# Performance work log

Measured on AMD Instinct MI355X. Metric: run time of the kernel, lower is better.

## Reference

```python
import jax, jax.numpy as jnp
import numpy as np
from jax import lax

BASE_LOWER, BASE_UPPER = 0.05, 0.2
WINDOW_SIZES = (11, 25, 49)
DN = ('NCHW', 'OIHW', 'NCHW')


def _conv3x3(x, w, b):
    y = lax.conv_general_dilated(x, w, (1, 1), [(1, 1), (1, 1)], dimension_numbers=DN)
    return y + b[None, :, None, None]


def _leaky(x):
    return jnp.where(x >= 0, x, 0.2 * x)


def _std_map(feats, ws):
    # box-filter local mean / mean-of-square via depthwise conv (same math as per-channel loop)
    N, C, H, W = feats.shape
    pad = ws // 2
    fp = jnp.pad(feats, ((0, 0), (0, 0), (pad, pad), (pad, pad)), mode='reflect')
    k = jnp.ones((C, 1, ws, ws), feats.dtype) / (ws * ws)
    mean = lax.conv_general_dilated(fp, k, (1, 1), 'VALID', dimension_numbers=DN, feature_group_count=C)
    mean_sq = lax.conv_general_dilated(fp * fp, k, (1, 1), 'VALID', dimension_numbers=DN, feature_group_count=C)
    var = jnp.clip(mean_sq - mean * mean, 1e-6, None)
    cw = jax.nn.softmax(jnp.ones((C,), feats.dtype))  # C=8 -> uniform 1/8
    res = jnp.sum(jnp.sqrt(var) * cw[None, :, None, None], axis=1, keepdims=True)  # [N,1,H,W]
    return jnp.power(res, 0.8)


def _segmented_sigmoid(ns):
    low = jax.nn.sigmoid(10.0 * ns - 1.5) * 0.4
    mid = jax.nn.sigmoid(20.0 * ns - 8.0) * 0.5 + 0.25
    high = jax.nn.sigmoid(8.0 * ns - 1.0) * 0.3 + 0.7
    return jnp.where(ns < 0.25, low, jnp.where(ns <= 0.6, mid, high))


def _forward(x, w1, b1, w2, b2, w3, b3, wf, bf, channel_weights):
    # feature extractor: 4->32->16->8
    f = _conv3x3(x, w1, b1)
    f = _leaky(f)
    f = _conv3x3(f, w2, b2)
    f = _leaky(f)
    f = _conv3x3(f, w3, b3)  # [B,8,H,W]

    maps = [_std_map(f, ws) for ws in WINDOW_SIZES]
    multi = jnp.concatenate(maps, axis=1)  # [B,3,H,W]
    fused = lax.conv_general_dilated(multi, wf, (1, 1), 'VALID', dimension_numbers=DN) + bf[None, :, None, None]
    fused = jnp.maximum(fused, 0.0)  # [B,1,H,W]

    # adaptive thresholds (torch.std -> ddof=1)
    g_std = jnp.std(x, axis=(2, 3), keepdims=True, ddof=1)
    g_fac = jnp.clip(g_std * 5.0, 0.5, 2.0)
    lt = BASE_LOWER * g_fac
    ut = BASE_UPPER * g_fac
    cw = jax.nn.softmax(channel_weights).reshape(1, -1, 1, 1)
    c_std = jnp.std(x * cw, axis=(2, 3), keepdims=True, ddof=1)
    c_fac = jnp.clip(c_std * 2.0, 0.8, 1.2)
    lt = lt * c_fac  # [B,4,1,1]
    ut = ut * c_fac

    # mask generation
    q_low = jnp.quantile(fused.reshape(-1), 0.3)
    q_high = jnp.quantile(fused.reshape(-1), 0.7)
    l_mean = jnp.mean(lt, axis=1, keepdims=True)
    u_mean = jnp.mean(ut, axis=1, keepdims=True)
    l_th = (l_mean + q_low) / 2
    u_th = (u_mean + q_high) / 2
    u_th = jnp.where(u_th - l_th < 0.01, l_th + 0.01, u_th)
    ns = jnp.clip((fused - l_th) / (u_th - l_th), 0.0, 1.0)
    return _segmented_sigmoid(ns)


def setup_inputs() -> dict:
    key = jax.random.key(0)
    ks = jax.random.split(key, 8)
    B, C, H, W = 1, 4, 1536, 1536
    x = jax.random.normal(ks[0], (B, C, H, W), jnp.float32)
    w1 = jax.random.normal(ks[1], (32, 4, 3, 3), jnp.float32) * 0.1
    b1 = jax.random.normal(ks[2], (32,), jnp.float32) * 0.01
    w2 = jax.random.normal(ks[3], (16, 32, 3, 3), jnp.float32) * 0.1
    b2 = jax.random.normal(ks[4], (16,), jnp.float32) * 0.01
    w3 = jax.random.normal(ks[5], (8, 16, 3, 3), jnp.float32) * 0.1
    b3 = jax.random.normal(ks[6], (8,), jnp.float32) * 0.01
    wf = jnp.full((1, 3, 1, 1), 1.0 / 3.0, jnp.float32)  # scale_fusion init
    bf = jnp.zeros((1,), jnp.float32)
    channel_weights = jnp.ones((4,), jnp.float32) / 4.0
    return {"x": x, "w1": w1, "b1": b1, "w2": w2, "b2": b2, "w3": w3, "b3": b3,
            "wf": wf, "bf": bf, "channel_weights": channel_weights}


def reference(x, w1, b1, w2, b2, w3, b3, wf, bf, channel_weights):
    return _forward(x, w1, b1, w2, b2, w3, b3, wf, bf, channel_weights)
```

## Files before the change

kernel.cpp:

```cpp
#include <hip/hip_runtime.h>
#include <math.h>

#define HH 1536
#define WW 1536
#define HWSZ (HH*WW)

typedef __attribute__((ext_vector_type(8))) short bf16x8;
typedef __attribute__((ext_vector_type(4))) float f32x4;
#define MFMA16 __builtin_amdgcn_mfma_f32_16x16x32_bf16

struct Scalars {
  float gsum[4];
  float gsumsq[4];
};

#define OFF_F3    0UL
#define OFF_FUSED 75497472UL
#define OFF_SC    84934656UL
#define OFF_GHA   (OFF_SC + 1024UL)
#define OFF_GHB   (OFF_GHA + 2048UL*4UL)
#define OFF_GHC   (OFF_GHB + 4UL*2048UL*4UL)
#define OFF_WP    (OFF_GHC + 4UL*1024UL*4UL)
#define WS_NEEDED (OFF_WP + 38UL*512UL*2UL)

__device__ __forceinline__ short f2bf(float f) {
  unsigned u = __float_as_uint(f);
  unsigned r = (u + 0x7FFFu + ((u >> 16) & 1u)) >> 16;
  return (short)(unsigned short)r;
}
__device__ __forceinline__ float bf2f(short s) {
  return __uint_as_float(((unsigned)(unsigned short)s) << 16);
}
__device__ __forceinline__ void tsplit(float v, short &h, short &l) {
  unsigned u = __float_as_uint(v);
  h = (short)(u >> 16);
  float r = v - __uint_as_float(u & 0xffff0000u);
  l = (short)(__float_as_uint(r) >> 16);
}
__device__ __forceinline__ float leaky_f(float v) { return v >= 0.f ? v : 0.2f*v; }

__global__ __launch_bounds__(256) void k_pack(const float* __restrict__ w1,
    const float* __restrict__ w2, const float* __restrict__ w3, short* __restrict__ wp) {
  int idx = blockIdx.x*256 + threadIdx.x;
  if (idx >= 38*512) return;
  int blk = idx >> 9, e = idx & 511;
  int oc = e >> 5, k = e & 31;
  float v = 0.f; int plane = 0;
  if (blk < 8) {
    plane = blk & 1; int sl = (blk >> 1) & 1, half = blk >> 2;
    int pos = sl*8 + (k >> 2), ic = k & 3;
    if (pos < 9) v = w1[((16*half + oc)*4 + ic)*9 + pos];
  } else if (blk < 28) {
    int t = blk - 8; plane = t & 1; int hs = t >> 1;
    int half = hs / 5, sl = hs % 5;
    int p = k >> 4, icl = k & 15;
    int pos = 2*sl + p;
    if (pos < 9) v = w2[(oc*32 + half*16 + icl)*9 + pos];
  } else {
    int t = blk - 28; plane = t & 1; int sl = t >> 1;
    int pos = 2*sl + (k >> 4), ic = k & 15;
    if (oc < 8 && pos < 9) v = w3[(oc*16 + ic)*9 + pos];
  }
  short h = f2bf(v);
  wp[idx] = plane ? f2bf(v - bf2f(h)) : h;
}

__global__ __launch_bounds__(256, 3) void k_conv(
    const float* __restrict__ x,
    const float* __restrict__ b1, const float* __restrict__ b2, const float* __restrict__ b3,
    const short* __restrict__ wp, float* __restrict__ f3, Scalars* __restrict__ sc)
{
  __shared__ __align__(16) short smem[23168];
  __shared__ float red[32];
  short* f1h  = smem;
  short* f1l  = smem + 6400;
  short* xs_h = smem + 12800;
  short* xs_l = smem + 14736;
  short* f2h  = smem + 12800;
  short* f2l  = smem + 17984;

  const int tid  = threadIdx.x;
  const int lane = tid & 63;
  const int wv   = tid >> 6;
  const int pl   = lane & 15;
  const int g    = lane >> 4;
  const int x0 = blockIdx.x * 16, y0 = blockIdx.y * 16;

  float st[8];
  #pragma unroll
  for (int k = 0; k < 8; ++k) st[k] = 0.f;
  for (int i = tid; i < 484; i += 256) {
    int ry = i / 22, rx = i % 22;
    int gy = y0 - 3 + ry, gx = x0 - 3 + rx;
    bool ok = ((unsigned)gy < HH) && ((unsigned)gx < WW);
    bool interior = (ry >= 3) && (ry < 19) && (rx >= 3) && (rx < 19);
    int off = gy*WW + gx;
    short4 hv, lv;
    #pragma unroll
    for (int ic = 0; ic < 4; ++ic) {
      float v = ok ? x[ic*HWSZ + off] : 0.f;
      if (interior) { st[ic*2] += v; st[ic*2+1] += v*v; }
      short h, l; tsplit(v, h, l);
      ((short*)&hv)[ic] = h;
      ((short*)&lv)[ic] = l;
    }
    *(short4*)&xs_h[i*4] = hv;
    *(short4*)&xs_l[i*4] = lv;
  }
  #pragma unroll
  for (int k = 0; k < 8; ++k) {
    for (int o = 32; o; o >>= 1) st[k] += __shfl_down(st[k], o, 64);
  }
  if (lane == 0) {
    #pragma unroll
    for (int k = 0; k < 8; ++k) red[wv*8 + k] = st[k];
  }
  __syncthreads();
  if (tid < 8) {
    float t = red[tid] + red[8+tid] + red[16+tid] + red[24+tid];
    int ch = tid >> 1;
    if (tid & 1) atomicAdd(&sc->gsumsq[ch], t);
    else         atomicAdd(&sc->gsum[ch],   t);
  }

  int c1ry[7], c1rx[7];
  #pragma unroll
  for (int n = 0; n < 7; ++n) {
    int G = wv + 4*n; if (G > 24) G = 24;
    int px = 16*G + pl;
    c1ry[n] = px / 20; c1rx[n] = px % 20;
  }
  int ryA[6], rxA[6];
  #pragma unroll
  for (int n = 0; n < 6; ++n) {
    int G = wv + 4*n; if (G > 20) G = 20;
    int px = 16*G + pl; if (px > 323) px = 323;
    ryA[n] = px / 18; rxA[n] = px % 18;
  }

  f32x4 acc2[6];
  {
    float4 bb = *(const float4*)&b2[4*g];
    #pragma unroll
    for (int n = 0; n < 6; ++n) acc2[n] = f32x4{bb.x, bb.y, bb.z, bb.w};
  }

  auto conv1_half = [&](int half) {
    f32x4 acc[7];
    float4 bb = *(const float4*)&b1[16*half + 4*g];
    #pragma unroll
    for (int n = 0; n < 7; ++n) acc[n] = f32x4{bb.x, bb.y, bb.z, bb.w};
    for (int sl = 0; sl < 2; ++sl) {
      const short* wb = wp + (size_t)((half*2 + sl)*2)*512;
      bf16x8 wh = *(const bf16x8*)(wb + pl*32 + 8*g);
      bf16x8 wl = *(const bf16x8*)(wb + 512 + pl*32 + 8*g);
      if (sl == 0) {
        int p0 = 2*g, p1 = 2*g + 1;
        int dy0 = p0/3, dx0 = p0%3, dy1 = p1/3, dx1 = p1%3;
        #pragma unroll
        for (int n = 0; n < 7; ++n) {
          int i0 = (c1ry[n] + dy0)*22 + c1rx[n] + dx0;
          int i1 = (c1ry[n] + dy1)*22 + c1rx[n] + dx1;
          short4 h0 = *(const short4*)&xs_h[i0*4];
          short4 h1 = *(const short4*)&xs_h[i1*4];
          short4 l0 = *(const short4*)&xs_l[i0*4];
          short4 l1 = *(const short4*)&xs_l[i1*4];
          bf16x8 bh = {h0.x,h0.y,h0.z,h0.w,h1.x,h1.y,h1.z,h1.w};
          bf16x8 bl = {l0.x,l0.y,l0.z,l0.w,l1.x,l1.y,l1.z,l1.w};
          acc[n] = MFMA16(wh, bh, acc[n], 0,0,0);
          acc[n] = MFMA16(wh, bl, acc[n], 0,0,0);
          acc[n] = MFMA16(wl, bh, acc[n], 0,0,0);
        }
      } else {
        #pragma unroll
        for (int n = 0; n < 7; ++n) {
          short4 h8 = {0,0,0,0}, l8 = {0,0,0,0};
          if (g == 0) {
            int i8 = (c1ry[n] + 2)*22 + c1rx[n] + 2;
            h8 = *(const short4*)&xs_h[i8*4];
            l8 = *(const short4*)&xs_l[i8*4];
          }
          bf16x8 bh = {h8.x,h8.y,h8.z,h8.w,0,0,0,0};
          bf16x8 bl = {l8.x,l8.y,l8.z,l8.w,0,0,0,0};
          acc[n] = MFMA16(wh, bh, acc[n], 0,0,0);
          acc[n] = MFMA16(wh, bl, acc[n], 0,0,0);
          acc[n] = MFMA16(wl, bh, acc[n], 0,0,0);
        }
      }
    }
    #pragma unroll
    for (int n = 0; n < 7; ++n) {
      int G = wv + 4*n; if (G > 24) G = 24;
      int px = 16*G + pl;
      int gy = y0 - 2 + c1ry[n], gx = x0 - 2 + c1rx[n];
      bool ok = ((unsigned)gy < HH) && ((unsigned)gx < WW);
      short4 hv, lv;
      #pragma unroll
      for (int r = 0; r < 4; ++r) {
        float v = ok ? leaky_f(acc[n][r]) : 0.f;
        short h, l; tsplit(v, h, l);
        ((short*)&hv)[r] = h;
        ((short*)&lv)[r] = l;
      }
      int fo = (g>>1)*3200 + px*8 + (g&1)*4;
      *(short4*)&f1h[fo] = hv;
      *(short4*)&f1l[fo] = lv;
    }
  };

  auto conv2_part = [&](int half) {
    for (int s = 0; s < 5; ++s) {
      const short* wb = wp + (size_t)(8 + (half*5 + s)*2)*512;
      bf16x8 wh = *(const bf16x8*)(wb + pl*32 + 8*g);
      bf16x8 wl = *(const bf16x8*)(wb + 512 + pl*32 + 8*g);
      int pos = 2*s + (g >> 1);
      bool pv = pos < 9;
      int dy = pv ? pos/3 : 0, dx = pv ? pos%3 : 0;
      const int pb = (g&1)*3200;
      #pragma unroll
      for (int n = 0; n < 6; ++n) {
        int idx = (ryA[n] + dy)*20 + rxA[n] + dx;
        bf16x8 bh = {0,0,0,0,0,0,0,0}, bl = {0,0,0,0,0,0,0,0};
        if (pv) {
          int so = pb + idx*8;
          bh = *(const bf16x8*)&f1h[so];
          bl = *(const bf16x8*)&f1l[so];
        }
        acc2[n] = MFMA16(wh, bh, acc2[n], 0,0,0);
        acc2[n] = MFMA16(wh, bl, acc2[n], 0,0,0);
        acc2[n] = MFMA16(wl, bh, acc2[n], 0,0,0);
      }
    }
  };

  conv1_half(0);
  __syncthreads();
  conv2_part(0);
  __syncthreads();
  conv1_half(1);
  __syncthreads();
  conv2_part(1);
  #pragma unroll
  for (int n = 0; n < 6; ++n) {
    int G = wv + 4*n; if (G > 20) G = 20;
    int px = 16*G + pl;
    if (px < 324) {
      int gy = y0 - 1 + ryA[n], gx = x0 - 1 + rxA[n];
      bool ok = ((unsigned)gy < HH) && ((unsigned)gx < WW);
      short4 hv, lv;
      #pragma unroll
      for (int r = 0; r < 4; ++r) {
        float v = ok ? leaky_f(acc2[n][r]) : 0.f;
        short h, l; tsplit(v, h, l);
        ((short*)&hv)[r] = h;
        ((short*)&lv)[r] = l;
      }
      int fo = (g>>1)*2592 + px*8 + (g&1)*4;
      *(short4*)&f2h[fo] = hv;
      *(short4*)&f2l[fo] = lv;
    }
  }
  __syncthreads();

  {
    f32x4 acc[4];
    float4 bb;
    if (g < 2) bb = *(const float4*)&b3[4*g];
    else { bb.x = 0.f; bb.y = 0.f; bb.z = 0.f; bb.w = 0.f; }
    #pragma unroll
    for (int n = 0; n < 4; ++n) acc[n] = f32x4{bb.x, bb.y, bb.z, bb.w};
    for (int s = 0; s < 5; ++s) {
      const short* wb = wp + (size_t)(28 + s*2)*512;
      bf16x8 wh = *(const bf16x8*)(wb + pl*32 + 8*g);
      bf16x8 wl = *(const bf16x8*)(wb + 512 + pl*32 + 8*g);
      int pos = 2*s + (g >> 1);
      bool pv = pos < 9;
      int dy = pv ? pos/3 : 0, dx = pv ? pos%3 : 0;
      const int pb = (g&1)*2592;
      #pragma unroll
      for (int n = 0; n < 4; ++n) {
        int px = 16*(wv + 4*n) + pl;
        int ry = px >> 4, rx = px & 15;
        int idx = (ry + dy)*18 + rx + dx;
        bf16x8 bh = {0,0,0,0,0,0,0,0}, bl = {0,0,0,0,0,0,0,0};
        if (pv) {
          int so = pb + idx*8;
          bh = *(const bf16x8*)&f2h[so];
          bl = *(const bf16x8*)&f2l[so];
        }
        acc[n] = MFMA16(wh, bh, acc[n], 0,0,0);
        acc[n] = MFMA16(wh, bl, acc[n], 0,0,0);
        acc[n] = MFMA16(wl, bh, acc[n], 0,0,0);
      }
    }
    #pragma unroll
    for (int n = 0; n < 4; ++n) {
      int px = 16*(wv + 4*n) + pl;
      int ry = px >> 4, rx = px & 15;
      size_t base = (size_t)(y0 + ry)*WW + (x0 + rx);
      #pragma unroll
      for (int r = 0; r < 4; ++r) {
        int oc = 4*g + r;
        if (oc < 8) f3[(size_t)oc*HWSZ + base] = acc[n][r];
      }
    }
  }
}

#define SATW 82
__device__ __forceinline__ float satv(const float* __restrict__ S, int r, int c) {
  return (r < 0 || c < 0) ? 0.f : S[r*SATW + c];
}
__device__ __forceinline__ float boxsum(const float* __restrict__ S, int r1, int r2, int c1, int c2) {
  return satv(S, r2, c2) - satv(S, r1-1, c2) - satv(S, r2, c1-1) + satv(S, r1-1, c1-1);
}

__global__ __launch_bounds__(256) void k_std(
    const float* __restrict__ f3, const float* __restrict__ wf,
    const float* __restrict__ bfp, float* __restrict__ fused, unsigned* __restrict__ ghA)
{
  __shared__ __align__(8) float S1[80*SATW];
  __shared__ __align__(8) float S2[80*SATW];
  const int tid = threadIdx.x;
  const int x0 = blockIdx.x * 32, y0 = blockIdx.y * 32;

  int off[25];
  #pragma unroll
  for (int it = 0; it < 25; ++it) {
    const int idx = tid + 256*it;
    const int r = idx / 80, cc = idx - r*80;
    int gy = y0 - 24 + r;  gy = gy < 0 ? -gy : (gy >= HH ? 2*HH - 2 - gy : gy);
    int gx = x0 - 24 + cc; gx = gx < 0 ? -gx : (gx >= WW ? 2*WW - 2 - gx : gx);
    off[it] = gy*WW + gx;
  }

  float pf[25];
  #pragma unroll
  for (int it = 0; it < 25; ++it) pf[it] = f3[off[it]];

  float acc0[4], acc1[4], acc2[4];
  #pragma unroll
  for (int k = 0; k < 4; ++k) { acc0[k] = 0.f; acc1[k] = 0.f; acc2[k] = 0.f; }

  for (int ch = 0; ch < 8; ++ch) {
    #pragma unroll
    for (int it = 0; it < 25; ++it) {
      const int idx = tid + 256*it;
      const int si = idx + 2*(idx/80);
      const float v = pf[it];
      S1[si] = v;
      S2[si] = v*v;
    }
    __syncthreads();
    if (ch < 7) {
      const float* fn = f3 + (size_t)(ch+1)*HWSZ;
      #pragma unroll
      for (int it = 0; it < 25; ++it) pf[it] = fn[off[it]];
    }
    if (tid < 160) {
      float* row = (tid >= 80 ? S2 + (tid-80)*SATW : S1 + tid*SATW);
      float run = 0.f;
      #pragma unroll
      for (int q = 0; q < 40; ++q) {
        float2 v = *(float2*)&row[q*2];
        float a = run + v.x;
        float b = a + v.y;
        float2 st = {a, b};
        *(float2*)&row[q*2] = st;
        run = b;
      }
    }
    __syncthreads();
    if (tid < 160) {
      float* Sc = (tid >= 80 ? S2 + (tid-80) : S1 + tid);
      float run = 0.f;
      #pragma unroll
      for (int g4 = 0; g4 < 20; ++g4) {
        float v0 = Sc[(g4*4+0)*SATW];
        float v1 = Sc[(g4*4+1)*SATW];
        float v2 = Sc[(g4*4+2)*SATW];
        float v3 = Sc[(g4*4+3)*SATW];
        run += v0; Sc[(g4*4+0)*SATW] = run;
        run += v1; Sc[(g4*4+1)*SATW] = run;
        run += v2; Sc[(g4*4+2)*SATW] = run;
        run += v3; Sc[(g4*4+3)*SATW] = run;
      }
    }
    __syncthreads();
    #pragma unroll
    for (int k = 0; k < 4; ++k) {
      const int px = tid + 256*k;
      const int py = px >> 5, xx = px & 31;
      {
        const float invn = 1.f/121.f;
        const float s1 = boxsum(S1, py+19, py+29, xx+19, xx+29);
        const float s2 = boxsum(S2, py+19, py+29, xx+19, xx+29);
        const float m = s1*invn;
        acc0[k] += sqrtf(fmaxf(s2*invn - m*m, 1e-6f));
      }
      {
        const float invn = 1.f/625.f;
        const float s1 = boxsum(S1, py+12, py+36, xx+12, xx+36);
        const float s2 = boxsum(S2, py+12, py+36, xx+12, xx+36);
        const float m = s1*invn;
        acc1[k] += sqrtf(fmaxf(s2*invn - m*m, 1e-6f));
      }
      {
        const float invn = 1.f/2401.f;
        const float s1 = boxsum(S1, py, py+48, xx, xx+48);
        const float s2 = boxsum(S2, py, py+48, xx, xx+48);
        const float m = s1*invn;
        acc2[k] += sqrtf(fmaxf(s2*invn - m*m, 1e-6f));
      }
    }
    __syncthreads();
  }

  unsigned* lh = (unsigned*)S1;
  for (int i = tid; i < 2048; i += 256) lh[i] = 0;
  __syncthreads();
  const float wv0 = wf[0], wv1 = wf[1], wv2 = wf[2], bv = bfp[0];
  #pragma unroll
  for (int k = 0; k < 4; ++k) {
    const int px = tid + 256*k;
    const int py = px >> 5, xx = px & 31;
    const float r0 = acc0[k]*0.125f, r1 = acc1[k]*0.125f, r2 = acc2[k]*0.125f;
    const float p0 = exp2f(0.8f*log2f(r0));
    const float p1 = exp2f(0.8f*log2f(r1));
    const float p2 = exp2f(0.8f*log2f(r2));
    float f = wv0*p0 + wv1*p1 + wv2*p2 + bv;
    f = fmaxf(f, 0.f);
    fused[(size_t)(y0 + py)*WW + (x0 + xx)] = f;
    atomicAdd(&lh[__float_as_uint(f) >> 21], 1u);
  }
  __syncthreads();
  for (int i = tid; i < 2048; i += 256) if (lh[i]) atomicAdd(&ghA[i], lh[i]);
}

__device__ bool scan_select(const unsigned* __restrict__ hist, int per, unsigned rank,
                            unsigned& bin, unsigned& inner) {
  const int lane = threadIdx.x & 63;
  const int base = lane * per;
  unsigned s = 0;
  for (int j = 0; j < per; ++j) s += hist[base + j];
  unsigned v = s;
  for (int off = 1; off < 64; off <<= 1) {
    unsigned n = __shfl_up(v, off, 64);
    if (lane >= off) v += n;
  }
  const unsigned excl = v - s;
  const bool has = (rank >= excl) && (rank < v);
  const unsigned long long m = __ballot(has);
  const int L = __ffsll(m) - 1;
  if (lane == L) {
    unsigned rem = rank - excl;
    for (int j = 0; j < per; ++j) {
      const unsigned c = hist[base + j];
      if (rem < c) { bin = (unsigned)(base + j); inner = rem; return true; }
      rem -= c;
    }
  }
  return false;
}

__global__ __launch_bounds__(256) void k_histB(const float* __restrict__ fused,
    const unsigned* __restrict__ ghA, unsigned* __restrict__ gh,
    unsigned r0, unsigned r1, unsigned r2, unsigned r3) {
  __shared__ unsigned lh[4*2048];
  __shared__ unsigned t1s[4];
  {
    const int w = threadIdx.x >> 6;
    const unsigned rk = (w == 0) ? r0 : (w == 1) ? r1 : (w == 2) ? r2 : r3;
    unsigned bin, inner;
    if (scan_select(ghA, 32, rk, bin, inner)) t1s[w] = bin;
  }
  for (int i = threadIdx.x; i < 8192; i += 256) lh[i] = 0;
  __syncthreads();
  const unsigned t0 = t1s[0], t1 = t1s[1], t2 = t1s[2], t3 = t1s[3];
  for (int i = blockIdx.x*256 + threadIdx.x; i < HWSZ; i += 512*256) {
    const unsigned u = __float_as_uint(fused[i]);
    const unsigned p = u >> 21, b = (u >> 10) & 2047u;
    if (p == t0) atomicAdd(&lh[b], 1u);
    if (p == t1) atomicAdd(&lh[2048 + b], 1u);
    if (p == t2) atomicAdd(&lh[4096 + b], 1u);
    if (p == t3) atomicAdd(&lh[6144 + b], 1u);
  }
  __syncthreads();
  for (int i = threadIdx.x; i < 8192; i += 256) if (lh[i]) atomicAdd(&gh[i], lh[i]);
}

__global__ __launch_bounds__(256) void k_histC(const float* __restrict__ fused,
    const unsigned* __restrict__ ghA, const unsigned* __restrict__ ghB,
    unsigned* __restrict__ gh, unsigned r0, unsigned r1, unsigned r2, unsigned r3) {
  __shared__ unsigned lh[4*1024];
  __shared__ unsigned t1s[4], in1s[4], t2s[4];
  const int w = threadIdx.x >> 6;
  {
    const unsigned rk = (w == 0) ? r0 : (w == 1) ? r1 : (w == 2) ? r2 : r3;
    unsigned bin, inner;
    if (scan_select(ghA, 32, rk, bin, inner)) { t1s[w] = bin; in1s[w] = inner; }
  }
  __syncthreads();
  {
    unsigned bin, inner;
    if (scan_select(ghB + w*2048, 32, in1s[w], bin, inner))
      t2s[w] = (t1s[w] << 11) | bin;
  }
  for (int i = threadIdx.x; i < 4096; i += 256) lh[i] = 0;
  __syncthreads();
  const unsigned t0 = t2s[0], t1 = t2s[1], t2 = t2s[2], t3 = t2s[3];
  for (int i = blockIdx.x*256 + threadIdx.x; i < HWSZ; i += 512*256) {
    const unsigned u = __float_as_uint(fused[i]);
    const unsigned p = u >> 10, b = u & 1023u;
    if (p == t0) atomicAdd(&lh[b], 1u);
    if (p == t1) atomicAdd(&lh[1024 + b], 1u);
    if (p == t2) atomicAdd(&lh[2048 + b], 1u);
    if (p == t3) atomicAdd(&lh[3072 + b], 1u);
  }
  __syncthreads();
  for (int i = threadIdx.x; i < 4096; i += 256) if (lh[i]) atomicAdd(&gh[i], lh[i]);
}

__device__ __forceinline__ float seg_sig(float ns) {
  ns = fminf(fmaxf(ns, 0.f), 1.f);
  float res;
  if (ns < 0.25f)      res = 0.4f / (1.f + expf(-(10.f*ns - 1.5f)));
  else if (ns <= 0.6f) res = 0.5f / (1.f + expf(-(20.f*ns - 8.f))) + 0.25f;
  else                 res = 0.3f / (1.f + expf(-(8.f*ns - 1.f))) + 0.7f;
  return res;
}

__global__ __launch_bounds__(256) void k_apply(const float* __restrict__ fused,
    const Scalars* __restrict__ sc, const float* __restrict__ cwp,
    const unsigned* __restrict__ ghA, const unsigned* __restrict__ ghB,
    const unsigned* __restrict__ ghC, float* __restrict__ out,
    unsigned r0, unsigned r1, unsigned r2, unsigned r3, float fr_lo, float fr_hi) {
  __shared__ unsigned t1s[4], in1s[4], t2s[4], in2s[4];
  __shared__ float vqs[4];
  __shared__ float ths[2];
  const int w = threadIdx.x >> 6;
  {
    const unsigned rk = (w == 0) ? r0 : (w == 1) ? r1 : (w == 2) ? r2 : r3;
    unsigned bin, inner;
    if (scan_select(ghA, 32, rk, bin, inner)) { t1s[w] = bin; in1s[w] = inner; }
  }
  __syncthreads();
  {
    unsigned bin, inner;
    if (scan_select(ghB + w*2048, 32, in1s[w], bin, inner)) {
      t2s[w] = (t1s[w] << 11) | bin; in2s[w] = inner;
    }
  }
  __syncthreads();
  {
    unsigned bin, inner;
    if (scan_select(ghC + w*1024, 16, in2s[w], bin, inner))
      vqs[w] = __uint_as_float((t2s[w] << 10) | bin);
  }
  __syncthreads();
  if (threadIdx.x == 0) {
    const float v0 = vqs[0], v1 = vqs[1], v2 = vqs[2], v3 = vqs[3];
    const float q_low  = v0 + fr_lo * (v1 - v0);
    const float q_high = v2 + fr_hi * (v3 - v2);
    const float c0 = cwp[0], c1 = cwp[1], c2 = cwp[2], c3 = cwp[3];
    const float mx = fmaxf(fmaxf(c0, c1), fmaxf(c2, c3));
    const float e0 = expf(c0 - mx), e1 = expf(c1 - mx), e2 = expf(c2 - mx), e3 = expf(c3 - mx);
    const float es = e0 + e1 + e2 + e3;
    const float cw[4] = {e0/es, e1/es, e2/es, e3/es};
    const double N = (double)HWSZ;
    float lsum = 0.f, usum = 0.f;
    for (int c = 0; c < 4; ++c) {
      double var = ((double)sc->gsumsq[c] - (double)sc->gsum[c]*(double)sc->gsum[c]/N) / (N - 1.0);
      if (var < 0.0) var = 0.0;
      const float gs = (float)sqrt(var);
      const float gf = fminf(fmaxf(gs*5.f, 0.5f), 2.f);
      float lt = 0.05f*gf, ut = 0.2f*gf;
      const float cs = cw[c]*gs;
      const float cf = fminf(fmaxf(cs*2.f, 0.8f), 1.2f);
      lt *= cf; ut *= cf;
      lsum += lt; usum += ut;
    }
    float l_th = 0.5f*(lsum*0.25f + q_low);
    float u_th = 0.5f*(usum*0.25f + q_high);
    if (u_th - l_th < 0.01f) u_th = l_th + 0.01f;
    ths[0] = l_th; ths[1] = u_th;
  }
  __syncthreads();
  const float l = ths[0], u = ths[1];
  const float d = u - l;
  const int i = blockIdx.x*256 + threadIdx.x;
  if (i < HWSZ/4) {
    const float4 v = ((const float4*)fused)[i];
    float4 r;
    r.x = seg_sig((v.x - l) / d);
    r.y = seg_sig((v.y - l) / d);
    r.z = seg_sig((v.z - l) / d);
    r.w = seg_sig((v.w - l) / d);
    ((float4*)out)[i] = r;
  }
}

extern "C" void kernel_launch(void* const* d_in, const int* in_sizes, int n_in,
                              void* d_out, int out_size, void* d_ws, size_t ws_size,
                              hipStream_t stream) {
  const float* x  = (const float*)d_in[0];
  const float* w1 = (const float*)d_in[1];
  const float* b1 = (const float*)d_in[2];
  const float* w2 = (const float*)d_in[3];
  const float* b2 = (const float*)d_in[4];
  const float* w3 = (const float*)d_in[5];
  const float* b3 = (const float*)d_in[6];
  const float* wf = (const float*)d_in[7];
  const float* bf = (const float*)d_in[8];
  const float* cw = (const float*)d_in[9];
  char* ws = (char*)d_ws;
  if (ws_size < WS_NEEDED) return;

  float*    f3    = (float*)(ws + OFF_F3);
  float*    fused = (float*)(ws + OFF_FUSED);
  Scalars*  sc    = (Scalars*)(ws + OFF_SC);
  unsigned* ghA   = (unsigned*)(ws + OFF_GHA);
  unsigned* ghB   = (unsigned*)(ws + OFF_GHB);
  unsigned* ghC   = (unsigned*)(ws + OFF_GHC);
  short*    wp    = (short*)(ws + OFF_WP);

  hipMemsetAsync(ws + OFF_SC, 0, OFF_WP - OFF_SC, stream);

  const double p_lo = 0.3 * (double)(HWSZ - 1);
  const double p_hi = 0.7 * (double)(HWSZ - 1);
  const unsigned k0 = (unsigned)p_lo, k1 = (unsigned)p_hi;
  const float fr_lo = (float)(p_lo - (double)k0);
  const float fr_hi = (float)(p_hi - (double)k1);

  k_pack <<<76, 256, 0, stream>>>(w1, w2, w3, wp);
  k_conv <<<dim3(96, 96), 256, 0, stream>>>(x, b1, b2, b3, wp, f3, sc);
  k_std  <<<dim3(48, 48), 256, 0, stream>>>(f3, wf, bf, fused, ghA);
  k_histB<<<512, 256, 0, stream>>>(fused, ghA, ghB, k0, k0 + 1, k1, k1 + 1);
  k_histC<<<512, 256, 0, stream>>>(fused, ghA, ghB, ghC, k0, k0 + 1, k1, k1 + 1);
  k_apply<<<(HWSZ/4 + 255)/256, 256, 0, stream>>>(fused, sc, cw, ghA, ghB, ghC,
      (float*)d_out, k0, k0 + 1, k1, k1 + 1, fr_lo, fr_hi);
}
```

Measured before the change: 483.4 us.

## Use a single shared SAT buffer in k_std, processing squares then values sequentially

The std-map kernel now keeps one 80x82 summed-area table in shared memory instead of two. For each channel it first builds the SAT of squared values, reads the three box sums into registers, then rebuilds the table from plain values to get the means. Shared memory per block is halved, and the 25-register prefetch of the next channel is dropped, which could allow more blocks per CU. In exchange each channel does two global gathers, twice as many scan passes with only 80 active threads, and more barriers, and loads are no longer overlapped with compute.

After: 672.9 us. 39.2% more time.

```diff
diff --git a/kernel.cpp b/kernel.cpp
--- a/kernel.cpp
+++ b/kernel.cpp
@@ -315,12 +315,44 @@
   return satv(S, r2, c2) - satv(S, r1-1, c2) - satv(S, r2, c1-1) + satv(S, r1-1, c1-1);
 }
 
+__device__ __forceinline__ void sat_scan(float* __restrict__ S, int tid) {
+  if (tid < 80) {
+    float* row = S + tid*SATW;
+    float run = 0.f;
+    #pragma unroll
+    for (int q = 0; q < 40; ++q) {
+      float2 v = *(float2*)&row[q*2];
+      float a = run + v.x;
+      float b = a + v.y;
+      float2 st = {a, b};
+      *(float2*)&row[q*2] = st;
+      run = b;
+    }
+  }
+  __syncthreads();
+  if (tid < 80) {
+    float* Sc = S + tid;
+    float run = 0.f;
+    #pragma unroll
+    for (int g4 = 0; g4 < 20; ++g4) {
+      float v0 = Sc[(g4*4+0)*SATW];
+      float v1 = Sc[(g4*4+1)*SATW];
+      float v2 = Sc[(g4*4+2)*SATW];
+      float v3 = Sc[(g4*4+3)*SATW];
+      run += v0; Sc[(g4*4+0)*SATW] = run;
+      run += v1; Sc[(g4*4+1)*SATW] = run;
+      run += v2; Sc[(g4*4+2)*SATW] = run;
+      run += v3; Sc[(g4*4+3)*SATW] = run;
+    }
+  }
+  __syncthreads();
+}
+
 __global__ __launch_bounds__(256) void k_std(
     const float* __restrict__ f3, const float* __restrict__ wf,
     const float* __restrict__ bfp, float* __restrict__ fused, unsigned* __restrict__ ghA)
 {
-  __shared__ __align__(8) float S1[80*SATW];
-  __shared__ __align__(8) float S2[80*SATW];
+  __shared__ __align__(8) float S[80*SATW];
   const int tid = threadIdx.x;
   const int x0 = blockIdx.x * 32, y0 = blockIdx.y * 32;
 
@@ -334,89 +366,63 @@
     off[it] = gy*WW + gx;
   }
 
-  float pf[25];
-  #pragma unroll
-  for (int it = 0; it < 25; ++it) pf[it] = f3[off[it]];
-
   float acc0[4], acc1[4], acc2[4];
   #pragma unroll
   for (int k = 0; k < 4; ++k) { acc0[k] = 0.f; acc1[k] = 0.f; acc2[k] = 0.f; }
 
   for (int ch = 0; ch < 8; ++ch) {
+    const float* fc = f3 + (size_t)ch * HWSZ;
     #pragma unroll
     for (int it = 0; it < 25; ++it) {
       const int idx = tid + 256*it;
       const int si = idx + 2*(idx/80);
-      const float v = pf[it];
-      S1[si] = v;
-      S2[si] = v*v;
+      const float v = fc[off[it]];
+      S[si] = v*v;
     }
     __syncthreads();
-    if (ch < 7) {
-      const float* fn = f3 + (size_t)(ch+1)*HWSZ;
-      #pragma unroll
-      for (int it = 0; it < 25; ++it) pf[it] = fn[off[it]];
-    }
-    if (tid < 160) {
-      float* row = (tid >= 80 ? S2 + (tid-80)*SATW : S1 + tid*SATW);
-      float run = 0.f;
-      #pragma unroll
-      for (int q = 0; q < 40; ++q) {
-        float2 v = *(float2*)&row[q*2];
-        float a = run + v.x;
-        float b = a + v.y;
-        float2 st = {a, b};
-        *(float2*)&row[q*2] = st;
-        run = b;
-      }
+    sat_scan(S, tid);
+    float q0[4], q1[4], q2[4];
+    #pragma unroll
+    for (int k = 0; k < 4; ++k) {
+      const int px = tid + 256*k;
+      const int py = px >> 5, xx = px & 31;
+      q0[k] = boxsum(S, py+19, py+29, xx+19, xx+29);
+      q1[k] = boxsum(S, py+12, py+36, xx+12, xx+36);
+      q2[k] = boxsum(S, py,    py+48, xx,    xx+48);
     }
     __syncthreads();
-    if (tid < 160) {
-      float* Sc = (tid >= 80 ? S2 + (tid-80) : S1 + tid);
-      float run = 0.f;
-      #pragma unroll
-      for (int g4 = 0; g4 < 20; ++g4) {
-        float v0 = Sc[(g4*4+0)*SATW];
-        float v1 = Sc[(g4*4+1)*SATW];
-        float v2 = Sc[(g4*4+2)*SATW];
-        float v3 = Sc[(g4*4+3)*SATW];
-        run += v0; Sc[(g4*4+0)*SATW] = run;
-        run += v1; Sc[(g4*4+1)*SATW] = run;
-        run += v2; Sc[(g4*4+2)*SATW] = run;
-        run += v3; Sc[(g4*4+3)*SATW] = run;
-      }
+    #pragma unroll
+    for (int it = 0; it < 25; ++it) {
+      const int idx = tid + 256*it;
+      const int si = idx + 2*(idx/80);
+      S[si] = fc[off[it]];
     }
     __syncthreads();
+    sat_scan(S, tid);
     #pragma unroll
     for (int k = 0; k < 4; ++k) {
       const int px = tid + 256*k;
       const int py = px >> 5, xx = px & 31;
       {
         const float invn = 1.f/121.f;
-        const float s1 = boxsum(S1, py+19, py+29, xx+19, xx+29);
-        const float s2 = boxsum(S2, py+19, py+29, xx+19, xx+29);
-        const float m = s1*invn;
-        acc0[k] += sqrtf(fmaxf(s2*invn - m*m, 1e-6f));
+        const float m = boxsum(S, py+19, py+29, xx+19, xx+29) * invn;
+        acc0[k] += sqrtf(fmaxf(q0[k]*invn - m*m, 1e-6f));
       }
       {
         const float invn = 1.f/625.f;
-        const float s1 = boxsum(S1, py+12, py+36, xx+12, xx+36);
-        const float s2 = boxsum(S2, py+12, py+36, xx+12, xx+36);
-        const float m = s1*invn;
-        acc1[k] += sqrtf(fmaxf(s2*invn - m*m, 1e-6f));
+        const float m = boxsum(S, py+12, py+36, xx+12, xx+36) * invn;
+        acc1[k] += sqrtf(fmaxf(q1[k]*invn - m*m, 1e-6f));
       }
       {
         const float invn = 1.f/2401.f;
-        const float s1 = boxsum(S1, py, py+48, xx, xx+48);
-        const float s2 = boxsum(S2, py, py+48, xx, xx+48);
-        const float m = s1*invn;
-        acc2[k] += sqrtf(fmaxf(s2*invn - m*m, 1e-6f));
+        const float m = boxsum(S, py, py+48, xx, xx+48) * invn;
+        acc2[k] += sqrtf(fmaxf(q2[k]*invn - m*m, 1e-6f));
       }
     }
     __syncthreads();
   }
 
-  unsigned* lh = (unsigned*)S1;
+  unsigned* lh = (unsigned*)S;
   for (int i = tid; i < 2048; i += 256) lh[i] = 0;
   __syncthreads();
   const float wv0 = wf[0], wv1 = wf[1], wv2 = wf[2], bv = bfp[0];
```

## Fuse histogram refinement and apply into one cooperative kernel; fold memset into pack

Applied to the files above, without the earlier changes.

Replaces the three tail kernels (histB, histC, apply) with a single cooperative kernel that uses grid-wide syncs between the radix-select histogram passes and the final sigmoid apply. The workspace memset is dropped and its zeroing is done inside the weight-pack kernel instead. This targets kernel launch gaps and the separate memset. In exchange it relies on cooperative launch with 1024 resident blocks using 32KB of LDS each, and falls back to the old three-kernel path if that launch fails.

Measured after the change: 638.9 us. 32.2% more time.

```diff
diff --git a/kernel.cpp b/kernel.cpp
--- a/kernel.cpp
+++ b/kernel.cpp
@@ -1,5 +1,8 @@
 #include <hip/hip_runtime.h>
+#include <hip/hip_cooperative_groups.h>
 #include <math.h>
+
+namespace cg = cooperative_groups;
 
 #define HH 1536
 #define WW 1536
@@ -22,6 +25,7 @@
 #define OFF_GHC   (OFF_GHB + 4UL*2048UL*4UL)
 #define OFF_WP    (OFF_GHC + 4UL*1024UL*4UL)
 #define WS_NEEDED (OFF_WP + 38UL*512UL*2UL)
+#define ZWORDS 14592
 
 __device__ __forceinline__ short f2bf(float f) {
   unsigned u = __float_as_uint(f);
@@ -40,8 +44,10 @@
 __device__ __forceinline__ float leaky_f(float v) { return v >= 0.f ? v : 0.2f*v; }
 
 __global__ __launch_bounds__(256) void k_pack(const float* __restrict__ w1,
-    const float* __restrict__ w2, const float* __restrict__ w3, short* __restrict__ wp) {
+    const float* __restrict__ w2, const float* __restrict__ w3, short* __restrict__ wp,
+    unsigned* __restrict__ zr) {
   int idx = blockIdx.x*256 + threadIdx.x;
+  if (idx < ZWORDS) zr[idx] = 0;
   if (idx >= 38*512) return;
   int blk = idx >> 9, e = idx & 511;
   int oc = e >> 5, k = e & 31;
@@ -463,6 +469,123 @@
   return false;
 }
 
+__device__ __forceinline__ float seg_sig(float ns) {
+  ns = fminf(fmaxf(ns, 0.f), 1.f);
+  float res;
+  if (ns < 0.25f)      res = 0.4f / (1.f + expf(-(10.f*ns - 1.5f)));
+  else if (ns <= 0.6f) res = 0.5f / (1.f + expf(-(20.f*ns - 8.f))) + 0.25f;
+  else                 res = 0.3f / (1.f + expf(-(8.f*ns - 1.f))) + 0.7f;
+  return res;
+}
+
+__device__ void tail_thresholds(const Scalars* sc, const float* cwp,
+    float q_low, float q_high, float* ths) {
+  const float c0 = cwp[0], c1 = cwp[1], c2 = cwp[2], c3 = cwp[3];
+  const float mx = fmaxf(fmaxf(c0, c1), fmaxf(c2, c3));
+  const float e0 = expf(c0 - mx), e1 = expf(c1 - mx), e2 = expf(c2 - mx), e3 = expf(c3 - mx);
+  const float es = e0 + e1 + e2 + e3;
+  const float cw[4] = {e0/es, e1/es, e2/es, e3/es};
+  const double N = (double)HWSZ;
+  float lsum = 0.f, usum = 0.f;
+  for (int c = 0; c < 4; ++c) {
+    double var = ((double)sc->gsumsq[c] - (double)sc->gsum[c]*(double)sc->gsum[c]/N) / (N - 1.0);
+    if (var < 0.0) var = 0.0;
+    const float gs = (float)sqrt(var);
+    const float gf = fminf(fmaxf(gs*5.f, 0.5f), 2.f);
+    float lt = 0.05f*gf, ut = 0.2f*gf;
+    const float cs = cw[c]*gs;
+    const float cf = fminf(fmaxf(cs*2.f, 0.8f), 1.2f);
+    lt *= cf; ut *= cf;
+    lsum += lt; usum += ut;
+  }
+  float l_th = 0.5f*(lsum*0.25f + q_low);
+  float u_th = 0.5f*(usum*0.25f + q_high);
+  if (u_th - l_th < 0.01f) u_th = l_th + 0.01f;
+  ths[0] = l_th; ths[1] = u_th;
+}
+
+__global__ __launch_bounds__(256) void k_tail(const float* __restrict__ fused,
+    const Scalars* __restrict__ sc, const float* __restrict__ cwp,
+    unsigned* __restrict__ ghA, unsigned* __restrict__ ghB, unsigned* __restrict__ ghC,
+    float* __restrict__ out,
+    unsigned r0, unsigned r1, unsigned r2, unsigned r3, float fr_lo, float fr_hi) {
+  cg::grid_group grid = cg::this_grid();
+  __shared__ unsigned lh[8192];
+  __shared__ unsigned t1s[4], in1s[4], t2s[4], in2s[4];
+  __shared__ float vqs[4], ths[2];
+  const int tid = threadIdx.x;
+  const int w = tid >> 6;
+  const unsigned rk = (w == 0) ? r0 : (w == 1) ? r1 : (w == 2) ? r2 : r3;
+
+  {
+    unsigned bin, inner;
+    if (scan_select(ghA, 32, rk, bin, inner)) { t1s[w] = bin; in1s[w] = inner; }
+  }
+  for (int i = tid; i < 8192; i += 256) lh[i] = 0;
+  __syncthreads();
+  {
+    const unsigned a0 = t1s[0], a1 = t1s[1], a2 = t1s[2], a3 = t1s[3];
+    for (int i = blockIdx.x*256 + tid; i < HWSZ; i += 1024*256) {
+      const unsigned u = __float_as_uint(fused[i]);
+      const unsigned p = u >> 21, b = (u >> 10) & 2047u;
+      if (p == a0) atomicAdd(&lh[b], 1u);
+      if (p == a1) atomicAdd(&lh[2048 + b], 1u);
+      if (p == a2) atomicAdd(&lh[4096 + b], 1u);
+      if (p == a3) atomicAdd(&lh[6144 + b], 1u);
+    }
+  }
+  __syncthreads();
+  for (int i = tid; i < 8192; i += 256) if (lh[i]) atomicAdd(&ghB[i], lh[i]);
+  grid.sync();
+
+  {
+    unsigned bin, inner;
+    if (scan_select(ghB + w*2048, 32, in1s[w], bin, inner)) {
+      t2s[w] = (t1s[w] << 11) | bin; in2s[w] = inner;
+    }
+  }
+  for (int i = tid; i < 4096; i += 256) lh[i] = 0;
+  __syncthreads();
+  {
+    const unsigned c0 = t2s[0], c1 = t2s[1], c2 = t2s[2], c3 = t2s[3];
+    for (int i = blockIdx.x*256 + tid; i < HWSZ; i += 1024*256) {
+      const unsigned u = __float_as_uint(fused[i]);
+      const unsigned p = u >> 10, b = u & 1023u;
+      if (p == c0) atomicAdd(&lh[b], 1u);
+      if (p == c1) atomicAdd(&lh[1024 + b], 1u);
+      if (p == c2) atomicAdd(&lh[2048 + b], 1u);
+      if (p == c3) atomicAdd(&lh[3072 + b], 1u);
+    }
+  }
+  __syncthreads();
+  for (int i = tid; i < 4096; i += 256) if (lh[i]) atomicAdd(&ghC[i], lh[i]);
+  grid.sync();
+
+  {
+    unsigned bin, inner;
+    if (scan_select(ghC + w*1024, 16, in2s[w], bin, inner))
+      vqs[w] = __uint_as_float((t2s[w] << 10) | bin);
+  }
+  __syncthreads();
+  if (tid == 0) {
+    const float q_low  = vqs[0] + fr_lo * (vqs[1] - vqs[0]);
+    const float q_high = vqs[2] + fr_hi * (vqs[3] - vqs[2]);
+    tail_thresholds(sc, cwp, q_low, q_high, ths);
+  }
+  __syncthreads();
+  const float l = ths[0], u = ths[1];
+  const float d = u - l;
+  for (int i = blockIdx.x*256 + tid; i < HWSZ/4; i += 1024*256) {
+    const float4 v = ((const float4*)fused)[i];
+    float4 r;
+    r.x = seg_sig((v.x - l) / d);
+    r.y = seg_sig((v.y - l) / d);
+    r.z = seg_sig((v.z - l) / d);
+    r.w = seg_sig((v.w - l) / d);
+    ((float4*)out)[i] = r;
+  }
+}
+
 __global__ __launch_bounds__(256) void k_histB(const float* __restrict__ fused,
     const unsigned* __restrict__ ghA, unsigned* __restrict__ gh,
     unsigned r0, unsigned r1, unsigned r2, unsigned r3) {
@@ -519,15 +642,6 @@
   }
   __syncthreads();
   for (int i = threadIdx.x; i < 4096; i += 256) if (lh[i]) atomicAdd(&gh[i], lh[i]);
-}
-
-__device__ __forceinline__ float seg_sig(float ns) {
-  ns = fminf(fmaxf(ns, 0.f), 1.f);
-  float res;
-  if (ns < 0.25f)      res = 0.4f / (1.f + expf(-(10.f*ns - 1.5f)));
-  else if (ns <= 0.6f) res = 0.5f / (1.f + expf(-(20.f*ns - 8.f))) + 0.25f;
-  else                 res = 0.3f / (1.f + expf(-(8.f*ns - 1.f))) + 0.7f;
-  return res;
 }
 
 __global__ __launch_bounds__(256) void k_apply(const float* __restrict__ fused,
@@ -559,31 +673,9 @@
   }
   __syncthreads();
   if (threadIdx.x == 0) {
-    const float v0 = vqs[0], v1 = vqs[1], v2 = vqs[2], v3 = vqs[3];
-    const float q_low  = v0 + fr_lo * (v1 - v0);
-    const float q_high = v2 + fr_hi * (v3 - v2);
-    const float c0 = cwp[0], c1 = cwp[1], c2 = cwp[2], c3 = cwp[3];
-    const float mx = fmaxf(fmaxf(c0, c1), fmaxf(c2, c3));
-    const float e0 = expf(c0 - mx), e1 = expf(c1 - mx), e2 = expf(c2 - mx), e3 = expf(c3 - mx);
-    const float es = e0 + e1 + e2 + e3;
-    const float cw[4] = {e0/es, e1/es, e2/es, e3/es};
-    const double N = (double)HWSZ;
-    float lsum = 0.f, usum = 0.f;
-    for (int c = 0; c < 4; ++c) {
-      double var = ((double)sc->gsumsq[c] - (double)sc->gsum[c]*(double)sc->gsum[c]/N) / (N - 1.0);
-      if (var < 0.0) var = 0.0;
-      const float gs = (float)sqrt(var);
-      const float gf = fminf(fmaxf(gs*5.f, 0.5f), 2.f);
-      float lt = 0.05f*gf, ut = 0.2f*gf;
-      const float cs = cw[c]*gs;
-      const float cf = fminf(fmaxf(cs*2.f, 0.8f), 1.2f);
-      lt *= cf; ut *= cf;
-      lsum += lt; usum += ut;
-    }
-    float l_th = 0.5f*(lsum*0.25f + q_low);
-    float u_th = 0.5f*(usum*0.25f + q_high);
-    if (u_th - l_th < 0.01f) u_th = l_th + 0.01f;
-    ths[0] = l_th; ths[1] = u_th;
+    const float q_low  = vqs[0] + fr_lo * (vqs[1] - vqs[0]);
+    const float q_high = vqs[2] + fr_hi * (vqs[3] - vqs[2]);
+    tail_thresholds(sc, cwp, q_low, q_high, ths);
   }
   __syncthreads();
   const float l = ths[0], u = ths[1];
@@ -623,20 +715,31 @@
   unsigned* ghB   = (unsigned*)(ws + OFF_GHB);
   unsigned* ghC   = (unsigned*)(ws + OFF_GHC);
   short*    wp    = (short*)(ws + OFF_WP);
-
-  hipMemsetAsync(ws + OFF_SC, 0, OFF_WP - OFF_SC, stream);
+  unsigned* zr    = (unsigned*)(ws + OFF_SC);
 
   const double p_lo = 0.3 * (double)(HWSZ - 1);
   const double p_hi = 0.7 * (double)(HWSZ - 1);
   const unsigned k0 = (unsigned)p_lo, k1 = (unsigned)p_hi;
-  const float fr_lo = (float)(p_lo - (double)k0);
-  const float fr_hi = (float)(p_hi - (double)k1);
-
-  k_pack <<<76, 256, 0, stream>>>(w1, w2, w3, wp);
+  float fr_lo = (float)(p_lo - (double)k0);
+  float fr_hi = (float)(p_hi - (double)k1);
+  unsigned r0 = k0, r1 = k0 + 1, r2 = k1, r3 = k1 + 1;
+
+  k_pack <<<76, 256, 0, stream>>>(w1, w2, w3, wp, zr);
   k_conv <<<dim3(96, 96), 256, 0, stream>>>(x, b1, b2, b3, wp, f3, sc);
   k_std  <<<dim3(48, 48), 256, 0, stream>>>(f3, wf, bf, fused, ghA);
-  k_histB<<<512, 256, 0, stream>>>(fused, ghA, ghB, k0, k0 + 1, k1, k1 + 1);
-  k_histC<<<512, 256, 0, stream>>>(fused, ghA, ghB, ghC, k0, k0 + 1, k1, k1 + 1);
-  k_apply<<<(HWSZ/4 + 255)/256, 256, 0, stream>>>(fused, sc, cw, ghA, ghB, ghC,
-      (float*)d_out, k0, k0 + 1, k1, k1 + 1, fr_lo, fr_hi);
-}
+
+  const float* fusedc = fused;
+  const Scalars* scc = sc;
+  float* outp = (float*)d_out;
+  void* args[] = {(void*)&fusedc, (void*)&scc, (void*)&cw, (void*)&ghA, (void*)&ghB,
+                  (void*)&ghC, (void*)&outp, (void*)&r0, (void*)&r1, (void*)&r2,
+                  (void*)&r3, (void*)&fr_lo, (void*)&fr_hi};
+  hipError_t e = hipLaunchCooperativeKernel((void*)k_tail, dim3(1024), dim3(256),
+                                            args, 0, stream);
+  if (e != hipSuccess) {
+    k_histB<<<512, 256, 0, stream>>>(fused, ghA, ghB, r0, r1, r2, r3);
+    k_histC<<<512, 256, 0, stream>>>(fused, ghA, ghB, ghC, r0, r1, r2, r3);
+    k_apply<<<(HWSZ/4 + 255)/256, 256, 0, stream>>>(fused, sc, cw, ghA, ghB, ghC,
+        outp, r0, r1, r2, r3, fr_lo, fr_hi);
+  }
+}
```
